# Performance work log

Measured on AMD Instinct MI355X. Metric: run time of the kernel, lower is better.

## Reference

```python
import jax, jax.numpy as jnp
import numpy as np

N_NODES = 50000
N_EDGES = 800000
N_GRAPHS = 256
FEAT = 128
HID = 64
HEADS = 4
OUT = 128
NEG_SLOPE = 0.2  # PyG GATConv default leaky_relu slope


def setup_inputs() -> dict:
    key = jax.random.key(0)
    ks = jax.random.split(key, 16)
    x = jax.random.normal(ks[0], (N_NODES, FEAT), dtype=jnp.float32)
    edge_index = jax.random.randint(ks[1], (2, N_EDGES), 0, N_NODES, dtype=jnp.int64)
    batch = jnp.sort(jax.random.randint(ks[2], (N_NODES,), 0, N_GRAPHS, dtype=jnp.int64))
    dims_in = [FEAT, HID * HEADS, HID * HEADS]
    params = {}
    for i, din in enumerate(dims_in):
        s = 1.0 / np.sqrt(din)
        params[f"W{i}"] = jax.random.normal(ks[3 + 4 * i], (din, HEADS * HID), dtype=jnp.float32) * s
        params[f"as{i}"] = jax.random.normal(ks[4 + 4 * i], (HEADS, HID), dtype=jnp.float32) * s
        params[f"ad{i}"] = jax.random.normal(ks[5 + 4 * i], (HEADS, HID), dtype=jnp.float32) * s
        params[f"b{i}"] = jnp.zeros((HEADS * HID,), dtype=jnp.float32)
    params["Wf"] = jax.random.normal(ks[15], (HID * HEADS, OUT), dtype=jnp.float32) / np.sqrt(HID * HEADS)
    params["bf"] = jnp.zeros((OUT,), dtype=jnp.float32)
    return {"x": x, "edge_index": edge_index, "batch": batch, **params}


def _gat_layer(x, src, dst, W, a_s, a_d, b):
    # x: [N, Din] -> h: [N, H, D]
    N = x.shape[0]
    h = (x @ W).reshape(N, HEADS, HID)
    alpha_src = jnp.einsum("nhd,hd->nh", h, a_s)  # [N, H]
    alpha_dst = jnp.einsum("nhd,hd->nh", h, a_d)
    e = jax.nn.leaky_relu(alpha_src[src] + alpha_dst[dst], NEG_SLOPE)  # [E, H]
    # segment softmax over edges sharing the same destination node
    m = jax.ops.segment_max(e, dst, num_segments=N)
    ex = jnp.exp(e - m[dst])
    s = jax.ops.segment_sum(ex, dst, num_segments=N)
    alpha = ex / s[dst]  # [E, H]
    msg = h[src] * alpha[:, :, None]  # [E, H, D]
    out = jax.ops.segment_sum(msg, dst, num_segments=N)  # [N, H, D]
    return out.reshape(N, HEADS * HID) + b


def reference(x, edge_index, batch, W0, as0, ad0, b0, W1, as1, ad1, b1,
              W2, as2, ad2, b2, Wf, bf):
    N = x.shape[0]
    loop = jnp.arange(N, dtype=edge_index.dtype)
    src = jnp.concatenate([edge_index[0], loop])  # PyG GATConv adds self-loops
    dst = jnp.concatenate([edge_index[1], loop])
    for W, a_s, a_d, b in ((W0, as0, ad0, b0), (W1, as1, ad1, b1), (W2, as2, ad2, b2)):
        x = jax.nn.elu(_gat_layer(x, src, dst, W, a_s, a_d, b))
    # global mean pool over graphs
    sums = jax.ops.segment_sum(x, batch, num_segments=N_GRAPHS)  # [G, HID*HEADS]
    cnt = jax.ops.segment_sum(jnp.ones((N,), x.dtype), batch, num_segments=N_GRAPHS)
    g = sums / jnp.maximum(cnt, 1.0)[:, None]
    y = g @ Wf + bf
    norm = jnp.linalg.norm(y, axis=-1, keepdims=True)
    return y / jnp.maximum(norm, 1e-12)
```

## Files before the change

kernel.cpp:

```cpp
#include <hip/hip_runtime.h>
#include <math.h>

#define NND 50000
#define NED 800000
#define ETOT 850000
#define NG 256
#define FEAT 128
#define CCH 256
#define OUTD 128
#define NEG 0.2f
#define NBLK 196
#define M2 50048

typedef __attribute__((ext_vector_type(8))) _Float16 half8;
typedef __attribute__((ext_vector_type(4))) _Float16 half4;
typedef __attribute__((ext_vector_type(4))) float floatx4;

#if __has_builtin(__builtin_amdgcn_global_load_lds)
#define GLOAD16(g, l) __builtin_amdgcn_global_load_lds( \
    (const __attribute__((address_space(1))) void*)(g), \
    (__attribute__((address_space(3))) void*)(l), 16, 0, 0)
#define HAVE_GLDS 1
#else
#define HAVE_GLDS 0
#endif


__global__ void zero_int_kernel(int* p, int n) {
    int i = blockIdx.x * 256 + threadIdx.x;
    if (i < n) p[i] = 0;
}

__global__ void count_kernel(const int* __restrict__ ei, int* __restrict__ deg) {
    int e = blockIdx.x * 256 + threadIdx.x;
    if (e >= ETOT) return;
    int dst = (e < NED) ? ei[NED + e] : (e - NED);
    atomicAdd(&deg[dst], 1);
}

__global__ __launch_bounds__(256) void scan_part_kernel(const int* __restrict__ deg,
                                                        int* __restrict__ bsum) {
    __shared__ int tile[256];
    int i = blockIdx.x * 256 + threadIdx.x;
    tile[threadIdx.x] = (i < NND) ? deg[i] : 0;
    __syncthreads();
    for (int s = 128; s > 0; s >>= 1) {
        if (threadIdx.x < s) tile[threadIdx.x] += tile[threadIdx.x + s];
        __syncthreads();
    }
    if (threadIdx.x == 0) bsum[blockIdx.x] = tile[0];
}

__global__ __launch_bounds__(256) void scan_bsum_kernel(int* __restrict__ bsum,
                                                        int* __restrict__ boff,
                                                        int* __restrict__ total) {
    __shared__ int tile[256];
    int t = threadIdx.x;
    int v = (t < NBLK) ? bsum[t] : 0;
    tile[t] = v;
    __syncthreads();
    for (int off = 1; off < 256; off <<= 1) {
        int u = (t >= off) ? tile[t - off] : 0;
        __syncthreads();
        tile[t] += u;
        __syncthreads();
    }
    if (t < NBLK) boff[t] = tile[t] - v;
    if (t == 255) *total = tile[255];
}

__global__ __launch_bounds__(256) void scan_write_kernel(const int* __restrict__ deg,
                                                         const int* __restrict__ boff,
                                                         const int* __restrict__ total,
                                                         int* __restrict__ rowptr,
                                                         int* __restrict__ cursor) {
    __shared__ int tile[256];
    int i = blockIdx.x * 256 + threadIdx.x;
    int t = threadIdx.x;
    int v = (i < NND) ? deg[i] : 0;
    tile[t] = v;
    __syncthreads();
    for (int off = 1; off < 256; off <<= 1) {
        int u = (t >= off) ? tile[t - off] : 0;
        __syncthreads();
        tile[t] += u;
        __syncthreads();
    }
    if (i < NND) {
        int r = boff[blockIdx.x] + tile[t] - v;
        rowptr[i] = r;
        cursor[i] = r;
    }
    if (i == 0) rowptr[NND] = *total;
}

__global__ void scatter_kernel(const int* __restrict__ ei, int* __restrict__ cursor,
                               int* __restrict__ csrsrc) {
    int e = blockIdx.x * 256 + threadIdx.x;
    if (e >= ETOT) return;
    int s, d;
    if (e < NED) { s = ei[e]; d = ei[NED + e]; } else { s = d = e - NED; }
    int pos = atomicAdd(&cursor[d], 1);
    csrsrc[pos] = s;
}


__global__ void decomp_x_kernel(const float4* __restrict__ x, half4* __restrict__ xo) {
    int i = blockIdx.x * 256 + threadIdx.x;
    if (i >= NND * FEAT / 4) return;
    float4 v = x[i];
    half4 o;
    o[0] = (_Float16)v.x; o[1] = (_Float16)v.y;
    o[2] = (_Float16)v.z; o[3] = (_Float16)v.w;
    xo[i] = o;
}

__global__ void wdecomp_all_kernel(const float* __restrict__ W0,
                                   const float* __restrict__ W1,
                                   const float* __restrict__ W2,
                                   _Float16* __restrict__ wt0,
                                   _Float16* __restrict__ wt1,
                                   _Float16* __restrict__ wt2) {
    int j = blockIdx.x * 256 + threadIdx.x;
    if (j < 256 * 128) {
        int n = j >> 7, k = j & 127;
        wt0[j] = (_Float16)W0[k * 256 + n];
        return;
    }
    j -= 256 * 128;
    if (j < 256 * 256) {
        int n = j >> 8, k = j & 255;
        wt1[j] = (_Float16)W1[k * 256 + n];
        return;
    }
    j -= 256 * 256;
    if (j < 256 * 256) {
        int n = j >> 8, k = j & 255;
        wt2[j] = (_Float16)W2[k * 256 + n];
    }
}


#define BK 64

__global__ __launch_bounds__(256, 3) void gemm_mfma_kernel(
        const _Float16* __restrict__ A,
        const _Float16* __restrict__ Bt,
        const float* __restrict__ as_, const float* __restrict__ ad_,
        _Float16* __restrict__ Hm,
        float* __restrict__ asrc, float* __restrict__ adst, int K) {
    __shared__ _Float16 AsF[128 * 64];
    __shared__ _Float16 BsF[128 * 64];
    const int t = threadIdx.x;
    const int bn = blockIdx.x * 128;
    const int bm = blockIdx.y * 128;
    const int lane = t & 63, wv = t >> 6;
    const int wm = (wv >> 1) * 64, wn = (wv & 1) * 64;
    const int fr = lane & 15, q = lane >> 4;

    floatx4 acc[4][4] = {};

    const int lrow = t >> 3;
    const int c8 = t & 7;

    for (int k0 = 0; k0 < K; k0 += BK) {
        for (int p = 0; p < 4; p++) {
            int row = p * 32 + lrow;
            int g8 = c8 ^ (row & 7);
            const _Float16* ga = A + (size_t)(bm + row) * K + k0 + g8 * 8;
            const _Float16* gb = Bt + (size_t)(bn + row) * K + k0 + g8 * 8;
#if HAVE_GLDS
            GLOAD16(ga, &AsF[row * 64 + c8 * 8]);
            GLOAD16(gb, &BsF[row * 64 + c8 * 8]);
#else
            *(half8*)&AsF[row * 64 + c8 * 8] = *(const half8*)ga;
            *(half8*)&BsF[row * 64 + c8 * 8] = *(const half8*)gb;
#endif
        }
        __syncthreads();
        for (int kc = 0; kc < 2; kc++) {
            half8 af[4], bf[4];
            int kb = kc * 4 + q;
            int cs = (kb ^ (fr & 7)) * 8;
            for (int mi = 0; mi < 4; mi++)
                af[mi] = *(const half8*)&AsF[(wm + mi * 16 + fr) * 64 + cs];
            for (int ni = 0; ni < 4; ni++)
                bf[ni] = *(const half8*)&BsF[(wn + ni * 16 + fr) * 64 + cs];
            for (int mi = 0; mi < 4; mi++)
                for (int ni = 0; ni < 4; ni++)
                    acc[mi][ni] = __builtin_amdgcn_mfma_f32_16x16x32_f16(
                        af[mi], bf[ni], acc[mi][ni], 0, 0, 0);
        }
        __syncthreads();
    }

    for (int mi = 0; mi < 4; mi++) {
        int row0 = bm + wm + mi * 16 + q * 4;
        for (int ni = 0; ni < 4; ni++) {
            int col = bn + wn + ni * 16 + fr;
            for (int r = 0; r < 4; r++)
                Hm[(size_t)(row0 + r) * CCH + col] = (_Float16)acc[mi][ni][r];
        }
    }

    const int hd = (bn + wn) >> 6;
    float asf[4], adf[4];
    for (int ni = 0; ni < 4; ni++) {
        asf[ni] = as_[hd * 64 + ni * 16 + fr];
        adf[ni] = ad_[hd * 64 + ni * 16 + fr];
    }
    for (int mi = 0; mi < 4; mi++)
        for (int r = 0; r < 4; r++) {
            float ps = 0.f, pd = 0.f;
            for (int ni = 0; ni < 4; ni++) {
                float v = acc[mi][ni][r];
                ps += v * asf[ni];
                pd += v * adf[ni];
            }
            for (int m = 1; m < 16; m <<= 1) {
                ps += __shfl_xor(ps, m, 64);
                pd += __shfl_xor(pd, m, 64);
            }
            if (fr == 0) {
                int row = bm + wm + mi * 16 + q * 4 + r;
                asrc[row * 4 + hd] = ps;
                adst[row * 4 + hd] = pd;
            }
        }
}


__global__ __launch_bounds__(256) void agg_kernel(const _Float16* __restrict__ H16,
                                                  const float* __restrict__ asrc,
                                                  const float* __restrict__ adst,
                                                  const int* __restrict__ rowptr,
                                                  const int* __restrict__ csrsrc,
                                                  const float4* __restrict__ bias4,
                                                  half8* __restrict__ xo) {
    int wave = threadIdx.x >> 6, lane = threadIdx.x & 63;
    int n = blockIdx.x * 4 + wave;
    if (n >= NND) return;
    int rs = rowptr[n], re = rowptr[n + 1];
    int hd = lane >> 4;
    int sub = lane & 15;
    int l32 = lane & 31;
    int myh = l32 >> 3;
    int epar = lane >> 5;
    float adv = adst[n * 4 + hd];
    float acc[8] = {};
    float ssum = 0.f;
    const _Float16* hb = H16 + l32 * 8;
    for (int e0 = rs; e0 < re; e0 += 16) {
        int sl = e0 + sub;
        bool ok = sl < re;
        int idxv = ok ? csrsrc[sl] : 0;
        float ev = 0.f;
        if (ok) {
            float a = asrc[idxv * 4 + hd] + adv;
            a = a > 0.f ? a : NEG * a;
            ev = __expf(a);
        }
        ssum += ev;
        int cnt = re - e0; if (cnt > 16) cnt = 16;
        #pragma unroll
        for (int j2 = 0; j2 < 8; j2++) {
            if (j2 * 2 >= cnt) break;
            int j = j2 * 2 + epar;
            int s = __shfl(idxv, j, 64);
            float ww = __shfl(ev, myh * 16 + j, 64);
            half8 hv = *(const half8*)&hb[(size_t)s * CCH];
            #pragma unroll
            for (int k = 0; k < 8; k++) acc[k] += ww * (float)hv[k];
        }
    }
    for (int off = 1; off < 16; off <<= 1) ssum += __shfl_xor(ssum, off, 64);
    float inv = 1.f / __shfl(ssum, myh * 16, 64);
    #pragma unroll
    for (int k = 0; k < 8; k++) acc[k] += __shfl_xor(acc[k], 32, 64);
    if (lane < 32) {
        float4 b0 = bias4[l32 * 2], b1 = bias4[l32 * 2 + 1];
        float o[8];
        o[0] = acc[0] * inv + b0.x; o[1] = acc[1] * inv + b0.y;
        o[2] = acc[2] * inv + b0.z; o[3] = acc[3] * inv + b0.w;
        o[4] = acc[4] * inv + b1.x; o[5] = acc[5] * inv + b1.y;
        o[6] = acc[6] * inv + b1.z; o[7] = acc[7] * inv + b1.w;
        half8 h;
        #pragma unroll
        for (int k = 0; k < 8; k++) {
            float v = o[k];
            v = v > 0.f ? v : expm1f(v);
            h[k] = (_Float16)v;
        }
        xo[(size_t)n * 32 + l32] = h;
    }
}


__global__ void bounds_kernel(const int* __restrict__ batch, int* __restrict__ gstart) {
    int i = blockIdx.x * 256 + threadIdx.x;
    if (i >= NND) return;
    int b = batch[i];
    int bp = (i == 0) ? -1 : batch[i - 1];
    for (int g = bp + 1; g <= b; ++g) gstart[g] = i;
    if (i == NND - 1) {
        for (int g = b + 1; g <= NG; ++g) gstart[g] = NND;
    }
}

__global__ __launch_bounds__(256) void poolfinal_kernel(const _Float16* __restrict__ xa,
                                                        const int* __restrict__ gstart,
                                                        const float* __restrict__ Wf,
                                                        const float* __restrict__ bfv,
                                                        float* __restrict__ out) {
    int g = blockIdx.x, t = threadIdx.x;
    __shared__ float gm[256];
    __shared__ float red[128];
    int s = gstart[g], e = gstart[g + 1];
    float acc = 0.f;
    for (int i = s; i < e; i++)
        acc += (float)xa[(size_t)i * CCH + t];
    int cnt = e - s;
    gm[t] = acc / (float)(cnt > 0 ? cnt : 1);
    __syncthreads();
    float a = 0.f;
    if (t < OUTD) {
        a = bfv[t];
        for (int k = 0; k < CCH; k++) a += gm[k] * Wf[k * OUTD + t];
        red[t] = a * a;
    }
    __syncthreads();
    for (int sft = 64; sft > 0; sft >>= 1) {
        if (t < sft) red[t] += red[t + sft];
        __syncthreads();
    }
    if (t < OUTD) out[g * OUTD + t] = a / fmaxf(sqrtf(red[0]), 1e-12f);
}


extern "C" void kernel_launch(void* const* d_in, const int* in_sizes, int n_in,
                              void* d_out, int out_size, void* d_ws, size_t ws_size,
                              hipStream_t stream) {
    const float* x     = (const float*)d_in[0];
    const int*   ei    = (const int*)d_in[1];
    const int*   batch = (const int*)d_in[2];
    const float* W[3]  = {(const float*)d_in[3], (const float*)d_in[7],  (const float*)d_in[11]};
    const float* As[3] = {(const float*)d_in[4], (const float*)d_in[8],  (const float*)d_in[12]};
    const float* Ad[3] = {(const float*)d_in[5], (const float*)d_in[9],  (const float*)d_in[13]};
    const float* Bb[3] = {(const float*)d_in[6], (const float*)d_in[10], (const float*)d_in[14]};
    const float* Wf    = (const float*)d_in[15];
    const float* bf    = (const float*)d_in[16];
    float* out = (float*)d_out;

    _Float16* H16   = (_Float16*)d_ws;
    _Float16* act16 = H16 + (size_t)M2 * CCH;
    _Float16* wt0   = act16 + (size_t)M2 * CCH;
    _Float16* wt1   = wt0 + 256 * 128;
    _Float16* wt2   = wt1 + 256 * 256;
    float* asrc  = (float*)(wt2 + 256 * 256);
    float* adst  = asrc + (size_t)M2 * 4;
    int* deg     = (int*)(adst + (size_t)M2 * 4);
    int* rowptr  = deg + (NND + 1);
    int* cursor  = rowptr + (NND + 1);
    int* csrsrc  = cursor + (NND + 1);
    int* gstart  = csrsrc + ETOT;
    int* bsum    = gstart + (NG + 1);
    int* boff    = bsum + NBLK;
    int* total   = boff + NBLK;

    _Float16* wt[3] = {wt0, wt1, wt2};

    zero_int_kernel<<<(NND + 1 + 255) / 256, 256, 0, stream>>>(deg, NND + 1);
    count_kernel<<<(ETOT + 255) / 256, 256, 0, stream>>>(ei, deg);
    scan_part_kernel<<<NBLK, 256, 0, stream>>>(deg, bsum);
    scan_bsum_kernel<<<1, 256, 0, stream>>>(bsum, boff, total);
    scan_write_kernel<<<NBLK, 256, 0, stream>>>(deg, boff, total, rowptr, cursor);
    scatter_kernel<<<(ETOT + 255) / 256, 256, 0, stream>>>(ei, cursor, csrsrc);
    bounds_kernel<<<(NND + 255) / 256, 256, 0, stream>>>(batch, gstart);

    decomp_x_kernel<<<(NND * FEAT / 4 + 255) / 256, 256, 0, stream>>>(
        (const float4*)x, (half4*)act16);
    wdecomp_all_kernel<<<(256 * (128 + 256 + 256) + 255) / 256, 256, 0, stream>>>(
        W[0], W[1], W[2], wt0, wt1, wt2);

    int K = FEAT;
    for (int l = 0; l < 3; l++) {
        dim3 g(2, M2 / 128);
        gemm_mfma_kernel<<<g, 256, 0, stream>>>(act16, wt[l], As[l], Ad[l], H16, asrc, adst, K);
        agg_kernel<<<(NND + 3) / 4, 256, 0, stream>>>(H16, asrc, adst, rowptr, csrsrc,
                                                      (const float4*)Bb[l], (half8*)act16);
        K = CCH;
    }

    poolfinal_kernel<<<NG, 256, 0, stream>>>(act16, gstart, Wf, bf, out);
}
```

Measured before the change: 524.2 us.

## Fuse prep kernels, load GEMM B operand directly, prefetch next edge chunk in aggregation

Merges the degree zeroing, graph-boundary, x conversion and weight transpose kernels into a single launch, which cuts launch count. The GEMM stops staging the weight tile in LDS and reads B fragments straight from global memory, relying on L1/L2 caching of the small weight matrix while halving LDS traffic. The aggregation kernel software-prefetches the next 16 CSR indices and attention logits so their latency overlaps with the current chunk's gather. The direct global B loads are uncoalesced per lane and may stall the MFMA loop.

```diff
diff --git a/kernel.cpp b/kernel.cpp
--- a/kernel.cpp
+++ b/kernel.cpp
@@ -11,6 +11,7 @@
 #define NEG 0.2f
 #define NBLK 196
 #define M2 50048
+#define XBLK 6250
 
 typedef __attribute__((ext_vector_type(8))) _Float16 half8;
 typedef __attribute__((ext_vector_type(4))) _Float16 half4;
@@ -25,11 +26,6 @@
 #define HAVE_GLDS 0
 #endif
 
-
-__global__ void zero_int_kernel(int* p, int n) {
-    int i = blockIdx.x * 256 + threadIdx.x;
-    if (i < n) p[i] = 0;
-}
 
 __global__ void count_kernel(const int* __restrict__ ei, int* __restrict__ deg) {
     int e = blockIdx.x * 256 + threadIdx.x;
@@ -105,23 +101,47 @@
 }
 
 
-__global__ void decomp_x_kernel(const float4* __restrict__ x, half4* __restrict__ xo) {
-    int i = blockIdx.x * 256 + threadIdx.x;
-    if (i >= NND * FEAT / 4) return;
-    float4 v = x[i];
-    half4 o;
-    o[0] = (_Float16)v.x; o[1] = (_Float16)v.y;
-    o[2] = (_Float16)v.z; o[3] = (_Float16)v.w;
-    xo[i] = o;
-}
-
-__global__ void wdecomp_all_kernel(const float* __restrict__ W0,
-                                   const float* __restrict__ W1,
-                                   const float* __restrict__ W2,
-                                   _Float16* __restrict__ wt0,
-                                   _Float16* __restrict__ wt1,
-                                   _Float16* __restrict__ wt2) {
-    int j = blockIdx.x * 256 + threadIdx.x;
+__global__ __launch_bounds__(256) void prep_kernel(const int* __restrict__ batch,
+                                                   int* __restrict__ deg,
+                                                   int* __restrict__ gstart,
+                                                   const float4* __restrict__ x,
+                                                   half4* __restrict__ xo,
+                                                   const float* __restrict__ W0,
+                                                   const float* __restrict__ W1,
+                                                   const float* __restrict__ W2,
+                                                   _Float16* __restrict__ wt0,
+                                                   _Float16* __restrict__ wt1,
+                                                   _Float16* __restrict__ wt2) {
+    int b = blockIdx.x;
+    if (b < 196) {
+        int i = b * 256 + threadIdx.x;
+        if (i < NND + 1) deg[i] = 0;
+        return;
+    }
+    b -= 196;
+    if (b < 196) {
+        int i = b * 256 + threadIdx.x;
+        if (i >= NND) return;
+        int bb = batch[i];
+        int bp = (i == 0) ? -1 : batch[i - 1];
+        for (int g = bp + 1; g <= bb; ++g) gstart[g] = i;
+        if (i == NND - 1)
+            for (int g = bb + 1; g <= NG; ++g) gstart[g] = NND;
+        return;
+    }
+    b -= 196;
+    if (b < XBLK) {
+        int i = b * 256 + threadIdx.x;
+        if (i >= NND * FEAT / 4) return;
+        float4 v = x[i];
+        half4 o;
+        o[0] = (_Float16)v.x; o[1] = (_Float16)v.y;
+        o[2] = (_Float16)v.z; o[3] = (_Float16)v.w;
+        xo[i] = o;
+        return;
+    }
+    b -= XBLK;
+    int j = b * 256 + threadIdx.x;
     if (j < 256 * 128) {
         int n = j >> 7, k = j & 127;
         wt0[j] = (_Float16)W0[k * 256 + n];
@@ -150,7 +170,6 @@
         _Float16* __restrict__ Hm,
         float* __restrict__ asrc, float* __restrict__ adst, int K) {
     __shared__ _Float16 AsF[128 * 64];
-    __shared__ _Float16 BsF[128 * 64];
     const int t = threadIdx.x;
     const int bn = blockIdx.x * 128;
     const int bm = blockIdx.y * 128;
@@ -168,24 +187,21 @@
             int row = p * 32 + lrow;
             int g8 = c8 ^ (row & 7);
             const _Float16* ga = A + (size_t)(bm + row) * K + k0 + g8 * 8;
-            const _Float16* gb = Bt + (size_t)(bn + row) * K + k0 + g8 * 8;
 #if HAVE_GLDS
             GLOAD16(ga, &AsF[row * 64 + c8 * 8]);
-            GLOAD16(gb, &BsF[row * 64 + c8 * 8]);
 #else
             *(half8*)&AsF[row * 64 + c8 * 8] = *(const half8*)ga;
-            *(half8*)&BsF[row * 64 + c8 * 8] = *(const half8*)gb;
 #endif
         }
         __syncthreads();
         for (int kc = 0; kc < 2; kc++) {
             half8 af[4], bf[4];
-            int kb = kc * 4 + q;
-            int cs = (kb ^ (fr & 7)) * 8;
+            int cs = ((kc * 4 + q) ^ (fr & 7)) * 8;
+            for (int ni = 0; ni < 4; ni++)
+                bf[ni] = *(const half8*)&Bt[(size_t)(bn + wn + ni * 16 + fr) * K
+                                            + k0 + kc * 32 + q * 8];
             for (int mi = 0; mi < 4; mi++)
                 af[mi] = *(const half8*)&AsF[(wm + mi * 16 + fr) * 64 + cs];
-            for (int ni = 0; ni < 4; ni++)
-                bf[ni] = *(const half8*)&BsF[(wn + ni * 16 + fr) * 64 + cs];
             for (int mi = 0; mi < 4; mi++)
                 for (int ni = 0; ni < 4; ni++)
                     acc[mi][ni] = __builtin_amdgcn_mfma_f32_16x16x32_f16(
@@ -250,17 +266,25 @@
     float acc[8] = {};
     float ssum = 0.f;
     const _Float16* hb = H16 + l32 * 8;
+
+    int sl = rs + sub;
+    bool ok = sl < re;
+    int idx = ok ? csrsrc[sl] : 0;
+    float aval = asrc[idx * 4 + hd];
+
     for (int e0 = rs; e0 < re; e0 += 16) {
-        int sl = e0 + sub;
-        bool ok = sl < re;
-        int idxv = ok ? csrsrc[sl] : 0;
         float ev = 0.f;
         if (ok) {
-            float a = asrc[idxv * 4 + hd] + adv;
+            float a = aval + adv;
             a = a > 0.f ? a : NEG * a;
             ev = __expf(a);
         }
         ssum += ev;
+        int idxv = idx;
+        int sl2 = e0 + 16 + sub;
+        bool ok2 = sl2 < re;
+        int idx2 = ok2 ? csrsrc[sl2] : 0;
+        float aval2 = asrc[idx2 * 4 + hd];
         int cnt = re - e0; if (cnt > 16) cnt = 16;
         #pragma unroll
         for (int j2 = 0; j2 < 8; j2++) {
@@ -272,6 +296,7 @@
             #pragma unroll
             for (int k = 0; k < 8; k++) acc[k] += ww * (float)hv[k];
         }
+        idx = idx2; aval = aval2; ok = ok2;
     }
     for (int off = 1; off < 16; off <<= 1) ssum += __shfl_xor(ssum, off, 64);
     float inv = 1.f / __shfl(ssum, myh * 16, 64);
@@ -295,17 +320,6 @@
     }
 }
 
-
-__global__ void bounds_kernel(const int* __restrict__ batch, int* __restrict__ gstart) {
-    int i = blockIdx.x * 256 + threadIdx.x;
-    if (i >= NND) return;
-    int b = batch[i];
-    int bp = (i == 0) ? -1 : batch[i - 1];
-    for (int g = bp + 1; g <= b; ++g) gstart[g] = i;
-    if (i == NND - 1) {
-        for (int g = b + 1; g <= NG; ++g) gstart[g] = NND;
-    }
-}
 
 __global__ __launch_bounds__(256) void poolfinal_kernel(const _Float16* __restrict__ xa,
                                                         const int* __restrict__ gstart,
@@ -369,18 +383,14 @@
 
     _Float16* wt[3] = {wt0, wt1, wt2};
 
-    zero_int_kernel<<<(NND + 1 + 255) / 256, 256, 0, stream>>>(deg, NND + 1);
+    prep_kernel<<<196 + 196 + XBLK + 640, 256, 0, stream>>>(
+        batch, deg, gstart, (const float4*)x, (half4*)act16,
+        W[0], W[1], W[2], wt0, wt1, wt2);
     count_kernel<<<(ETOT + 255) / 256, 256, 0, stream>>>(ei, deg);
     scan_part_kernel<<<NBLK, 256, 0, stream>>>(deg, bsum);
     scan_bsum_kernel<<<1, 256, 0, stream>>>(bsum, boff, total);
     scan_write_kernel<<<NBLK, 256, 0, stream>>>(deg, boff, total, rowptr, cursor);
     scatter_kernel<<<(ETOT + 255) / 256, 256, 0, stream>>>(ei, cursor, csrsrc);
-    bounds_kernel<<<(NND + 255) / 256, 256, 0, stream>>>(batch, gstart);
-
-    decomp_x_kernel<<<(NND * FEAT / 4 + 255) / 256, 256, 0, stream>>>(
-        (const float4*)x, (half4*)act16);
-    wdecomp_all_kernel<<<(256 * (128 + 256 + 256) + 255) / 256, 256, 0, stream>>>(
-        W[0], W[1], W[2], wt0, wt1, wt2);
 
     int K = FEAT;
     for (int l = 0; l < 3; l++) {
```

Measured after the change: 540.9 us. 1.03x slower.
